# Performance work log

Measured on AMD Instinct MI355X. Metric: run time of the kernel, lower is better.

## Reference

```python
import jax, jax.numpy as jnp
import numpy as np

N_CELL, N_TISSUE, H, NH = 200000, 2000, 256, 8
HD = H // NH
SCALE = HD ** -0.5
EPS = 1e-5


def _layernorm(x, g, b):
    m = jnp.mean(x, axis=-1, keepdims=True)
    v = jnp.mean((x - m) ** 2, axis=-1, keepdims=True)
    return (x - m) / jnp.sqrt(v + EPS) * g + b


def setup_inputs() -> dict:
    key = jax.random.key(0)
    ks = jax.random.split(key, 12)
    s = 0.02

    def lin(k):
        k1, k2 = jax.random.split(k)
        return (jax.random.normal(k1, (H, H), jnp.float32) * s,
                jax.random.normal(k2, (H,), jnp.float32) * s)

    Wq_bu, bq_bu = lin(ks[0])
    Wk_bu, bk_bu = lin(ks[1])
    Wv_bu, bv_bu = lin(ks[2])
    Wo_bu, bo_bu = lin(ks[3])
    Wv_td, bv_td = lin(ks[4])
    Wo_td, bo_td = lin(ks[5])
    return dict(
        cell_features=jax.random.normal(ks[6], (N_CELL, H), jnp.float32),
        tissue_features=jax.random.normal(ks[7], (N_TISSUE, H), jnp.float32),
        cluster_labels=jax.random.randint(ks[8], (N_CELL,), 0, N_TISSUE, dtype=jnp.int32),
        tissue_batch=jnp.zeros((N_TISSUE,), jnp.int32),
        Wq_bu=Wq_bu, bq_bu=bq_bu, Wk_bu=Wk_bu, bk_bu=bk_bu,
        Wv_bu=Wv_bu, bv_bu=bv_bu, Wo_bu=Wo_bu, bo_bu=bo_bu,
        Wv_td=Wv_td, bv_td=bv_td, Wo_td=Wo_td, bo_td=bo_td,
        ln_cell_g=jnp.ones((H,), jnp.float32), ln_cell_b=jnp.zeros((H,), jnp.float32),
        ln_tissue_g=jnp.ones((H,), jnp.float32), ln_tissue_b=jnp.zeros((H,), jnp.float32),
    )


def reference(cell_features, tissue_features, cluster_labels, tissue_batch,
              Wq_bu, bq_bu, Wk_bu, bk_bu, Wv_bu, bv_bu, Wo_bu, bo_bu,
              Wv_td, bv_td, Wo_td, bo_td,
              ln_cell_g, ln_cell_b, ln_tissue_g, ln_tissue_b):
    Nc = cell_features.shape[0]
    Nt = tissue_features.shape[0]

    # ---- bottom-up: each tissue node (1 query) attends over its cells (segment attention) ----
    Q = (tissue_features @ Wq_bu + bq_bu).reshape(Nt, NH, HD)   # [Nt, h, d]
    K = (cell_features @ Wk_bu + bk_bu).reshape(Nc, NH, HD)     # [Nc, h, d]
    V = (cell_features @ Wv_bu + bv_bu).reshape(Nc, NH, HD)     # [Nc, h, d]

    # per-cell score against its own cluster's tissue query
    scores = jnp.einsum('nhd,nhd->nh', K, Q[cluster_labels]) * SCALE  # [Nc, h]
    smax = jax.lax.stop_gradient(
        jax.ops.segment_max(scores, cluster_labels, num_segments=Nt))  # [Nt, h]
    ex = jnp.exp(scores - smax[cluster_labels])
    denom = jax.ops.segment_sum(ex, cluster_labels, num_segments=Nt)   # [Nt, h]
    w = ex / denom[cluster_labels]                                     # [Nc, h]
    attended = jax.ops.segment_sum(w[..., None] * V, cluster_labels,
                                   num_segments=Nt)                    # [Nt, h, d]
    attended = attended.reshape(Nt, H) @ Wo_bu + bo_bu

    counts = jax.ops.segment_sum(jnp.ones((Nc,), cell_features.dtype),
                                 cluster_labels, num_segments=Nt)
    tissue_updated = jnp.where(counts[:, None] > 0, attended, tissue_features)

    # ---- top-down: each cell attends to its single tissue token ----
    # softmax over a single key is identically 1, so q/k projections cancel:
    # attended_cell = out_proj(v_proj(tissue_updated[cluster]))
    td_per_tissue = (tissue_updated @ Wv_td + bv_td) @ Wo_td + bo_td   # [Nt, H]
    cell_updated = td_per_tissue[cluster_labels]                       # [Nc, H]

    cell_out = _layernorm(cell_features + cell_updated, ln_cell_g, ln_cell_b)
    tissue_out = _layernorm(tissue_features + tissue_updated, ln_tissue_g, ln_tissue_b)
    return (cell_out, tissue_out)
```

## Files before the change

### kernel.cpp

```cpp
#include <hip/hip_runtime.h>
#include <math.h>

#define NC 200000
#define NT 2000
#define HH 256
#define NH_ 8
#define SCALE 0.17677669529663687f
#define EPS 1e-5f
#define SLICE 128
#define PSLICES (NT + NC / SLICE + 1)
#define PSTRIDE 2056


__global__ void k_hist(const int* __restrict__ labels, int* __restrict__ counts) {
  int i = blockIdx.x * 256 + threadIdx.x;
  if (i < NC) atomicAdd(&counts[labels[i]], 1);
}

__global__ void k_scan(const int* __restrict__ counts, int* __restrict__ offsets,
                       int* __restrict__ soff, int* __restrict__ slice_t) {
  int tid = threadIdx.x;
  int base = tid * 32;
  int la[32], lb[32], scnt[32];
  int sa = 0, sb = 0;
  #pragma unroll
  for (int k = 0; k < 32; k++) {
    int idx = base + k;
    int v = (idx < NT) ? counts[idx] : 0;
    la[k] = sa; lb[k] = sb;
    scnt[k] = (v + SLICE - 1) / SLICE;
    sa += v; sb += scnt[k];
  }
  int ia_ = sa, ib_ = sb;
  #pragma unroll
  for (int d = 1; d < 64; d <<= 1) {
    int oa = __shfl_up(ia_, d, 64);
    int ob = __shfl_up(ib_, d, 64);
    if (tid >= d) { ia_ += oa; ib_ += ob; }
  }
  int ea = ia_ - sa, eb = ib_ - sb;
  #pragma unroll
  for (int k = 0; k < 32; k++) {
    int idx = base + k;
    if (idx < NT) {
      offsets[idx] = ea + la[k];
      soff[idx] = eb + lb[k];
      int st = eb + lb[k];
      for (int s2 = 0; s2 < scnt[k]; s2++) slice_t[st + s2] = idx;
    }
  }
  if (tid == 63) { offsets[NT] = ia_; soff[NT] = ib_; }
}

__global__ void k_scatter(const int* __restrict__ labels, const int* __restrict__ offsets,
                          int* __restrict__ cursor, int* __restrict__ cindex) {
  int i = blockIdx.x * 256 + threadIdx.x;
  if (i < NC) {
    int c = labels[i];
    int pos = offsets[c] + atomicAdd(&cursor[c], 1);
    cindex[pos] = i;
  }
}


__global__ __launch_bounds__(256) void k_gemm_bias(
    const float* __restrict__ A, const float* __restrict__ W,
    const float* __restrict__ bias, float* __restrict__ C, int M)
{
  __shared__ float Al[16][33];
  __shared__ float Wl[32][HH];
  int tid = threadIdx.x;
  int r0 = blockIdx.x * 16;
  float acc[16];
  #pragma unroll
  for (int r = 0; r < 16; r++) acc[r] = 0.f;
  for (int k0 = 0; k0 < HH; k0 += 32) {
    for (int e = tid; e < 16 * 32; e += 256) {
      int r = e >> 5, k = e & 31;
      int row = r0 + r;
      Al[r][k] = (row < M) ? A[(size_t)row * HH + k0 + k] : 0.f;
    }
    for (int e = tid; e < 32 * HH; e += 256) {
      int k = e >> 8, j = e & 255;
      Wl[k][j] = W[(size_t)(k0 + k) * HH + j];
    }
    __syncthreads();
    for (int k = 0; k < 32; k++) {
      float w = Wl[k][tid];
      #pragma unroll
      for (int r = 0; r < 16; r++) acc[r] += Al[r][k] * w;
    }
    __syncthreads();
  }
  float bj = bias[tid];
  #pragma unroll
  for (int r = 0; r < 16; r++) {
    int row = r0 + r;
    if (row < M) C[(size_t)row * HH + tid] = acc[r] + bj;
  }
}


__global__ __launch_bounds__(256) void k_qproj(
    const float* __restrict__ Q, const float* __restrict__ Wk,
    const float* __restrict__ bk, float* __restrict__ Qproj,
    float* __restrict__ bkq)
{
  __shared__ float Al[64][33];
  __shared__ float Bl[32][257];
  int h = blockIdx.x & 7, tb = blockIdx.x >> 3;
  int t0 = tb * 64;
  int tid = threadIdx.x;
  for (int e = tid; e < 64 * 32; e += 256) {
    int r = e >> 5, d = e & 31;
    int t = t0 + r;
    Al[r][d] = (t < NT) ? Q[(size_t)t * HH + h * 32 + d] * SCALE : 0.f;
  }
  for (int e = tid; e < 256 * 32; e += 256) {
    int j = e >> 5, d = e & 31;
    Bl[d][j] = Wk[(size_t)j * HH + h * 32 + d];
  }
  __syncthreads();
  float acc[64];
  #pragma unroll
  for (int r = 0; r < 64; r++) acc[r] = 0.f;
  for (int d = 0; d < 32; d++) {
    float b = Bl[d][tid];
    #pragma unroll
    for (int r = 0; r < 64; r++) acc[r] += Al[r][d] * b;
  }
  for (int r = 0; r < 64; r++) {
    int t = t0 + r;
    if (t < NT) Qproj[((size_t)t * NH_ + h) * HH + tid] = acc[r];
  }
  if (tid < 64) {
    int t = t0 + tid;
    if (t < NT) {
      float s = 0.f;
      #pragma unroll
      for (int d = 0; d < 32; d++) s += Al[tid][d] * bk[h * 32 + d];
      bkq[t * NH_ + h] = s;
    }
  }
}


__global__ __launch_bounds__(256) void k_cellslice(
    const float* __restrict__ cell, const int* __restrict__ cindex,
    const int* __restrict__ offsets, const int* __restrict__ soff,
    const int* __restrict__ slice_t,
    const float* __restrict__ Qproj, const float* __restrict__ bkq,
    float* __restrict__ Pbuf)
{
  __shared__ float qp[NH_][HH];
  __shared__ float e_lds[SLICE][NH_];
  __shared__ int   cidx[SLICE];
  __shared__ float cwlds[NH_][HH];
  __shared__ float red[4][NH_];
  __shared__ float bqs[NH_];

  int s = blockIdx.x;
  if (s >= soff[NT]) return;
  int t = slice_t[s];
  int l = s - soff[t];
  int c0 = offsets[t] + l * SLICE;
  int c1 = min(c0 + SLICE, offsets[t + 1]);
  int nc = c1 - c0;
  int ncp = (nc + 15) & ~15;

  int tid = threadIdx.x;
  int w = tid >> 6, lane = tid & 63, slot = lane >> 3, g = lane & 7;

  for (int e = tid; e < NH_ * HH / 4; e += 256)
    ((float4*)qp)[e] = ((const float4*)(Qproj + (size_t)t * NH_ * HH))[e];
  if (tid < SLICE) cidx[tid] = cindex[min(c0 + tid, c1 - 1)];
  if (tid < NH_) bqs[tid] = bkq[t * NH_ + tid];
  for (int e = tid; e < SLICE * NH_; e += 256) ((float*)e_lds)[e] = 0.f;
  __syncthreads();

  int nsweep = ncp >> 4;
  for (int j = w; j < nsweep; j += 4) {
    int ia = j * 16 + slot, ib = ia + 8;
    const float* rowa = cell + (size_t)cidx[ia] * HH + g * 4;
    const float* rowb = cell + (size_t)cidx[ib] * HH + g * 4;
    float pa[NH_], pb[NH_];
    #pragma unroll
    for (int h = 0; h < NH_; h++) { pa[h] = 0.f; pb[h] = 0.f; }
    float4 a0 = *reinterpret_cast<const float4*>(rowa);
    float4 b0 = *reinterpret_cast<const float4*>(rowb);
    #pragma unroll
    for (int k = 0; k < 8; k++) {
      float4 a1, b1;
      if (k < 7) {
        a1 = *reinterpret_cast<const float4*>(rowa + 32 * (k + 1));
        b1 = *reinterpret_cast<const float4*>(rowb + 32 * (k + 1));
      }
      #pragma unroll
      for (int h = 0; h < NH_; h++) {
        float4 q = *reinterpret_cast<const float4*>(&qp[h][g * 4 + 32 * k]);
        pa[h] += a0.x * q.x + a0.y * q.y + a0.z * q.z + a0.w * q.w;
        pb[h] += b0.x * q.x + b0.y * q.y + b0.z * q.z + b0.w * q.w;
      }
      a0 = a1; b0 = b1;
    }
    #pragma unroll
    for (int d = 1; d < 8; d <<= 1) {
      #pragma unroll
      for (int h = 0; h < NH_; h++) {
        pa[h] += __shfl_xor(pa[h], d, 64);
        pb[h] += __shfl_xor(pb[h], d, 64);
      }
    }
    if (g == 0) {
      if (ia < nc) {
        float ea[NH_];
        #pragma unroll
        for (int h = 0; h < NH_; h++) ea[h] = __expf(pa[h] + bqs[h]);
        *reinterpret_cast<float4*>(&e_lds[ia][0]) = make_float4(ea[0], ea[1], ea[2], ea[3]);
        *reinterpret_cast<float4*>(&e_lds[ia][4]) = make_float4(ea[4], ea[5], ea[6], ea[7]);
      }
      if (ib < nc) {
        float eb[NH_];
        #pragma unroll
        for (int h = 0; h < NH_; h++) eb[h] = __expf(pb[h] + bqs[h]);
        *reinterpret_cast<float4*>(&e_lds[ib][0]) = make_float4(eb[0], eb[1], eb[2], eb[3]);
        *reinterpret_cast<float4*>(&e_lds[ib][4]) = make_float4(eb[4], eb[5], eb[6], eb[7]);
      }
    }
  }
  __syncthreads();

  float cw[NH_][4];
  float dsum[NH_];
  #pragma unroll
  for (int h = 0; h < NH_; h++) {
    cw[h][0] = cw[h][1] = cw[h][2] = cw[h][3] = 0.f;
    dsum[h] = 0.f;
  }
  for (int i = w * 4; i < ncp; i += 16) {
    float4 xx[4];
    #pragma unroll
    for (int c = 0; c < 4; c++)
      xx[c] = *reinterpret_cast<const float4*>(&cell[(size_t)cidx[i + c] * HH + lane * 4]);
    #pragma unroll
    for (int c = 0; c < 4; c++) {
      float4 e0 = *reinterpret_cast<float4*>(&e_lds[i + c][0]);
      float4 e1 = *reinterpret_cast<float4*>(&e_lds[i + c][4]);
      float4 x = xx[c];
      cw[0][0] += e0.x * x.x; cw[0][1] += e0.x * x.y; cw[0][2] += e0.x * x.z; cw[0][3] += e0.x * x.w;
      cw[1][0] += e0.y * x.x; cw[1][1] += e0.y * x.y; cw[1][2] += e0.y * x.z; cw[1][3] += e0.y * x.w;
      cw[2][0] += e0.z * x.x; cw[2][1] += e0.z * x.y; cw[2][2] += e0.z * x.z; cw[2][3] += e0.z * x.w;
      cw[3][0] += e0.w * x.x; cw[3][1] += e0.w * x.y; cw[3][2] += e0.w * x.z; cw[3][3] += e0.w * x.w;
      cw[4][0] += e1.x * x.x; cw[4][1] += e1.x * x.y; cw[4][2] += e1.x * x.z; cw[4][3] += e1.x * x.w;
      cw[5][0] += e1.y * x.x; cw[5][1] += e1.y * x.y; cw[5][2] += e1.y * x.z; cw[5][3] += e1.y * x.w;
      cw[6][0] += e1.z * x.x; cw[6][1] += e1.z * x.y; cw[6][2] += e1.z * x.z; cw[6][3] += e1.z * x.w;
      cw[7][0] += e1.w * x.x; cw[7][1] += e1.w * x.y; cw[7][2] += e1.w * x.z; cw[7][3] += e1.w * x.w;
      dsum[0] += e0.x; dsum[1] += e0.y; dsum[2] += e0.z; dsum[3] += e0.w;
      dsum[4] += e1.x; dsum[5] += e1.y; dsum[6] += e1.z; dsum[7] += e1.w;
    }
  }
  if (lane == 0) {
    #pragma unroll
    for (int h = 0; h < NH_; h++) red[w][h] = dsum[h];
  }
  if (w == 0) {
    #pragma unroll
    for (int h = 0; h < NH_; h++)
      *reinterpret_cast<float4*>(&cwlds[h][lane * 4]) =
          make_float4(cw[h][0], cw[h][1], cw[h][2], cw[h][3]);
  }
  __syncthreads();
  #pragma unroll
  for (int ww = 1; ww < 4; ww++) {
    if (w == ww) {
      #pragma unroll
      for (int h = 0; h < NH_; h++) {
        float4 c = *reinterpret_cast<float4*>(&cwlds[h][lane * 4]);
        c.x += cw[h][0]; c.y += cw[h][1]; c.z += cw[h][2]; c.w += cw[h][3];
        *reinterpret_cast<float4*>(&cwlds[h][lane * 4]) = c;
      }
    }
    __syncthreads();
  }

  float* pb = Pbuf + (size_t)s * PSTRIDE;
  #pragma unroll
  for (int h = 0; h < NH_; h++) pb[h * HH + tid] = cwlds[h][tid];
  if (tid < NH_) pb[2048 + tid] = red[0][tid] + red[1][tid] + red[2][tid] + red[3][tid];
}


#define TCH 4

__global__ __launch_bounds__(256) void k_tissuechain(
    const float* __restrict__ tissue, const int* __restrict__ counts,
    const float* __restrict__ Pbuf, const int* __restrict__ soff,
    const float* __restrict__ Wv, const float* __restrict__ bv,
    const float* __restrict__ Wo, const float* __restrict__ bo,
    const float* __restrict__ Wvtd, const float* __restrict__ bvtd,
    const float* __restrict__ Wotd, const float* __restrict__ botd,
    const float* __restrict__ lng, const float* __restrict__ lnb,
    float* __restrict__ td, float* __restrict__ out_tissue)
{
  __shared__ float s_cwn[TCH][NH_ * HH];
  __shared__ float s_a[TCH][HH];
  __shared__ float s_tu[TCH][HH];
  __shared__ float s_tmp[TCH][HH];
  __shared__ float s_red[2][4];
  __shared__ float s_dinv[TCH][NH_];
  int t0 = blockIdx.x * TCH;
  int j = threadIdx.x;
  int h = j >> 5;

  if (j < TCH * NH_) {
    int t = j >> 3, hh = j & 7;
    int s0 = soff[t0 + t], s1 = soff[t0 + t + 1];
    float d = 0.f;
    for (int q = s0; q < s1; q++) d += Pbuf[(size_t)q * PSTRIDE + 2048 + hh];
    s_dinv[t][hh] = (s1 > s0) ? 1.f / d : 0.f;
  }
  __syncthreads();

  for (int e = j; e < TCH * NH_ * HH; e += 256) {
    int t = e >> 11, c = e & 2047, hh = c >> 8;
    int s0 = soff[t0 + t], s1 = soff[t0 + t + 1];
    float a = 0.f;
    for (int q = s0; q < s1; q++) a += Pbuf[(size_t)q * PSTRIDE + c];
    s_cwn[t][c] = a * s_dinv[t][hh];
  }
  __syncthreads();

  float acc[TCH];
  #pragma unroll
  for (int t = 0; t < TCH; t++) acc[t] = 0.f;
  for (int k = 0; k < HH; k++) {
    float w = Wv[(size_t)k * HH + j];
    #pragma unroll
    for (int t = 0; t < TCH; t++) acc[t] += s_cwn[t][h * HH + k] * w;
  }
  {
    float bj = bv[j];
    #pragma unroll
    for (int t = 0; t < TCH; t++) s_a[t][j] = acc[t] + bj;
  }
  __syncthreads();

  #pragma unroll
  for (int t = 0; t < TCH; t++) acc[t] = 0.f;
  for (int k = 0; k < HH; k++) {
    float w = Wo[(size_t)k * HH + j];
    #pragma unroll
    for (int t = 0; t < TCH; t++) acc[t] += s_a[t][k] * w;
  }
  {
    float bj = bo[j];
    #pragma unroll
    for (int t = 0; t < TCH; t++) {
      int tt = t0 + t;
      s_tu[t][j] = (counts[tt] > 0) ? (acc[t] + bj) : tissue[(size_t)tt * HH + j];
    }
  }
  __syncthreads();

  #pragma unroll
  for (int t = 0; t < TCH; t++) acc[t] = 0.f;
  for (int k = 0; k < HH; k++) {
    float w = Wvtd[(size_t)k * HH + j];
    #pragma unroll
    for (int t = 0; t < TCH; t++) acc[t] += s_tu[t][k] * w;
  }
  {
    float bj = bvtd[j];
    #pragma unroll
    for (int t = 0; t < TCH; t++) s_tmp[t][j] = acc[t] + bj;
  }
  __syncthreads();

  #pragma unroll
  for (int t = 0; t < TCH; t++) acc[t] = 0.f;
  for (int k = 0; k < HH; k++) {
    float w = Wotd[(size_t)k * HH + j];
    #pragma unroll
    for (int t = 0; t < TCH; t++) acc[t] += s_tmp[t][k] * w;
  }
  {
    float bj = botd[j];
    #pragma unroll
    for (int t = 0; t < TCH; t++) td[(size_t)(t0 + t) * HH + j] = acc[t] + bj;
  }

  float gj = lng[j], bj2 = lnb[j];
  for (int t = 0; t < TCH; t++) {
    float y = tissue[(size_t)(t0 + t) * HH + j] + s_tu[t][j];
    float s1 = y, s2 = y * y;
    #pragma unroll
    for (int d = 1; d < 64; d <<= 1) { s1 += __shfl_xor(s1, d, 64); s2 += __shfl_xor(s2, d, 64); }
    int wv_ = j >> 6, ln_ = j & 63;
    __syncthreads();
    if (ln_ == 0) { s_red[0][wv_] = s1; s_red[1][wv_] = s2; }
    __syncthreads();
    s1 = s_red[0][0] + s_red[0][1] + s_red[0][2] + s_red[0][3];
    s2 = s_red[1][0] + s_red[1][1] + s_red[1][2] + s_red[1][3];
    float mean = s1 * (1.f / 256.f);
    float var = s2 * (1.f / 256.f) - mean * mean;
    float inv = rsqrtf(var + EPS);
    out_tissue[(size_t)(t0 + t) * HH + j] = (y - mean) * inv * gj + bj2;
  }
}


#define COB 2048

__global__ __launch_bounds__(256) void k_cellout(
    const float* __restrict__ cell, const float* __restrict__ td,
    const int* __restrict__ labels,
    const float* __restrict__ lng, const float* __restrict__ lnb,
    float* __restrict__ out)
{
  int lane = threadIdx.x & 63;
  float4 gv = *reinterpret_cast<const float4*>(&lng[lane * 4]);
  float4 bv = *reinterpret_cast<const float4*>(&lnb[lane * 4]);
  int wid = blockIdx.x * 4 + (threadIdx.x >> 6);
  for (int row = wid; row < NC; row += COB * 4) {
    int c = labels[row];
    float4 x = *reinterpret_cast<const float4*>(&cell[(size_t)row * HH + lane * 4]);
    float4 u = *reinterpret_cast<const float4*>(&td[(size_t)c * HH + lane * 4]);
    float y0 = x.x + u.x, y1 = x.y + u.y, y2 = x.z + u.z, y3 = x.w + u.w;
    float s1 = y0 + y1 + y2 + y3;
    float s2 = y0 * y0 + y1 * y1 + y2 * y2 + y3 * y3;
    #pragma unroll
    for (int d = 1; d < 64; d <<= 1) { s1 += __shfl_xor(s1, d, 64); s2 += __shfl_xor(s2, d, 64); }
    float mean = s1 * (1.f / 256.f);
    float var = s2 * (1.f / 256.f) - mean * mean;
    float inv = rsqrtf(var + EPS);
    float4 o;
    o.x = (y0 - mean) * inv * gv.x + bv.x;
    o.y = (y1 - mean) * inv * gv.y + bv.y;
    o.z = (y2 - mean) * inv * gv.z + bv.z;
    o.w = (y3 - mean) * inv * gv.w + bv.w;
    *reinterpret_cast<float4*>(&out[(size_t)row * HH + lane * 4]) = o;
  }
}


extern "C" void kernel_launch(void* const* d_in, const int* in_sizes, int n_in,
                              void* d_out, int out_size, void* d_ws, size_t ws_size,
                              hipStream_t stream) {
  const float* cell   = (const float*)d_in[0];
  const float* tissue = (const float*)d_in[1];
  const int*   labels = (const int*)d_in[2];
  const float* Wq = (const float*)d_in[4];  const float* bq = (const float*)d_in[5];
  const float* Wk = (const float*)d_in[6];  const float* bk = (const float*)d_in[7];
  const float* Wv = (const float*)d_in[8];  const float* bv = (const float*)d_in[9];
  const float* Wo = (const float*)d_in[10]; const float* bo = (const float*)d_in[11];
  const float* Wvtd = (const float*)d_in[12]; const float* bvtd = (const float*)d_in[13];
  const float* Wotd = (const float*)d_in[14]; const float* botd = (const float*)d_in[15];
  const float* lncg = (const float*)d_in[16]; const float* lncb = (const float*)d_in[17];
  const float* lntg = (const float*)d_in[18]; const float* lntb = (const float*)d_in[19];
  float* out_cell   = (float*)d_out;
  float* out_tissue = (float*)d_out + (size_t)NC * HH;

  char* w = (char*)d_ws;
  auto take = [&](size_t bytes) { void* p = (void*)w; w += (bytes + 255) & ~(size_t)255; return p; };
  int*   counts  = (int*)take((size_t)NT * 4);
  int*   cursor  = (int*)take((size_t)NT * 4);
  int*   offsets = (int*)take((size_t)(NT + 1) * 4);
  int*   soff    = (int*)take((size_t)(NT + 1) * 4);
  int*   slice_t = (int*)take((size_t)PSLICES * 4);
  int*   cindex  = (int*)take((size_t)NC * 4);
  float* Q       = (float*)take((size_t)NT * HH * 4);
  float* Qproj   = (float*)take((size_t)NT * NH_ * HH * 4);
  float* bkq     = (float*)take((size_t)NT * NH_ * 4);
  float* td      = (float*)take((size_t)NT * HH * 4);
  float* Pbuf    = (float*)take((size_t)PSLICES * PSTRIDE * 4);

  hipMemsetAsync(counts, 0, 16384, stream);

  const int CB = (NC + 255) / 256;
  k_hist<<<CB, 256, 0, stream>>>(labels, counts);
  k_scan<<<1, 64, 0, stream>>>(counts, offsets, soff, slice_t);
  k_scatter<<<CB, 256, 0, stream>>>(labels, offsets, cursor, cindex);

  k_gemm_bias<<<(NT + 15) / 16, 256, 0, stream>>>(tissue, Wq, bq, Q, NT);
  k_qproj<<<8 * ((NT + 63) / 64), 256, 0, stream>>>(Q, Wk, bk, Qproj, bkq);

  k_cellslice<<<PSLICES, 256, 0, stream>>>(cell, cindex, offsets, soff, slice_t,
                                           Qproj, bkq, Pbuf);

  k_tissuechain<<<NT / TCH, 256, 0, stream>>>(tissue, counts, Pbuf, soff,
      Wv, bv, Wo, bo, Wvtd, bvtd, Wotd, botd, lntg, lntb, td, out_tissue);

  k_cellout<<<COB, 256, 0, stream>>>(cell, td, labels, lncg, lncb, out_cell);
}
```

Baseline: 457.1 us.

## Fuse score and weighted-sum passes in cell slice kernel into one pass

```diff
diff --git a/kernel.cpp b/kernel.cpp
--- a/kernel.cpp
+++ b/kernel.cpp
@@ -152,12 +152,9 @@
     const float* __restrict__ Qproj, const float* __restrict__ bkq,
     float* __restrict__ Pbuf)
 {
-  __shared__ float qp[NH_][HH];
-  __shared__ float e_lds[SLICE][NH_];
   __shared__ int   cidx[SLICE];
   __shared__ float cwlds[NH_][HH];
   __shared__ float red[4][NH_];
-  __shared__ float bqs[NH_];
 
   int s = blockIdx.x;
   if (s >= soff[NT]) return;
@@ -166,118 +163,95 @@
   int c0 = offsets[t] + l * SLICE;
   int c1 = min(c0 + SLICE, offsets[t + 1]);
   int nc = c1 - c0;
-  int ncp = (nc + 15) & ~15;
+  int ncp = (nc + 3) & ~3;
 
   int tid = threadIdx.x;
-  int w = tid >> 6, lane = tid & 63, slot = lane >> 3, g = lane & 7;
-
-  for (int e = tid; e < NH_ * HH / 4; e += 256)
-    ((float4*)qp)[e] = ((const float4*)(Qproj + (size_t)t * NH_ * HH))[e];
+  int w = tid >> 6, lane = tid & 63;
+  int hg = lane & 3, kc = lane >> 2;
+
   if (tid < SLICE) cidx[tid] = cindex[min(c0 + tid, c1 - 1)];
-  if (tid < NH_) bqs[tid] = bkq[t * NH_ + tid];
-  for (int e = tid; e < SLICE * NH_; e += 256) ((float*)e_lds)[e] = 0.f;
-  __syncthreads();
-
-  int nsweep = ncp >> 4;
-  for (int j = w; j < nsweep; j += 4) {
-    int ia = j * 16 + slot, ib = ia + 8;
-    const float* rowa = cell + (size_t)cidx[ia] * HH + g * 4;
-    const float* rowb = cell + (size_t)cidx[ib] * HH + g * 4;
-    float pa[NH_], pb[NH_];
-    #pragma unroll
-    for (int h = 0; h < NH_; h++) { pa[h] = 0.f; pb[h] = 0.f; }
-    float4 a0 = *reinterpret_cast<const float4*>(rowa);
-    float4 b0 = *reinterpret_cast<const float4*>(rowb);
-    #pragma unroll
-    for (int k = 0; k < 8; k++) {
-      float4 a1, b1;
-      if (k < 7) {
-        a1 = *reinterpret_cast<const float4*>(rowa + 32 * (k + 1));
-        b1 = *reinterpret_cast<const float4*>(rowb + 32 * (k + 1));
-      }
-      #pragma unroll
-      for (int h = 0; h < NH_; h++) {
-        float4 q = *reinterpret_cast<const float4*>(&qp[h][g * 4 + 32 * k]);
-        pa[h] += a0.x * q.x + a0.y * q.y + a0.z * q.z + a0.w * q.w;
-        pb[h] += b0.x * q.x + b0.y * q.y + b0.z * q.z + b0.w * q.w;
-      }
-      a0 = a1; b0 = b1;
-    }
-    #pragma unroll
-    for (int d = 1; d < 8; d <<= 1) {
-      #pragma unroll
-      for (int h = 0; h < NH_; h++) {
-        pa[h] += __shfl_xor(pa[h], d, 64);
-        pb[h] += __shfl_xor(pb[h], d, 64);
-      }
-    }
-    if (g == 0) {
-      if (ia < nc) {
-        float ea[NH_];
-        #pragma unroll
-        for (int h = 0; h < NH_; h++) ea[h] = __expf(pa[h] + bqs[h]);
-        *reinterpret_cast<float4*>(&e_lds[ia][0]) = make_float4(ea[0], ea[1], ea[2], ea[3]);
-        *reinterpret_cast<float4*>(&e_lds[ia][4]) = make_float4(ea[4], ea[5], ea[6], ea[7]);
-      }
-      if (ib < nc) {
-        float eb[NH_];
-        #pragma unroll
-        for (int h = 0; h < NH_; h++) eb[h] = __expf(pb[h] + bqs[h]);
-        *reinterpret_cast<float4*>(&e_lds[ib][0]) = make_float4(eb[0], eb[1], eb[2], eb[3]);
-        *reinterpret_cast<float4*>(&e_lds[ib][4]) = make_float4(eb[4], eb[5], eb[6], eb[7]);
-      }
-    }
-  }
-  __syncthreads();
-
-  float cw[NH_][4];
-  float dsum[NH_];
-  #pragma unroll
-  for (int h = 0; h < NH_; h++) {
-    cw[h][0] = cw[h][1] = cw[h][2] = cw[h][3] = 0.f;
-    dsum[h] = 0.f;
-  }
-  for (int i = w * 4; i < ncp; i += 16) {
-    float4 xx[4];
-    #pragma unroll
-    for (int c = 0; c < 4; c++)
-      xx[c] = *reinterpret_cast<const float4*>(&cell[(size_t)cidx[i + c] * HH + lane * 4]);
-    #pragma unroll
-    for (int c = 0; c < 4; c++) {
-      float4 e0 = *reinterpret_cast<float4*>(&e_lds[i + c][0]);
-      float4 e1 = *reinterpret_cast<float4*>(&e_lds[i + c][4]);
-      float4 x = xx[c];
-      cw[0][0] += e0.x * x.x; cw[0][1] += e0.x * x.y; cw[0][2] += e0.x * x.z; cw[0][3] += e0.x * x.w;
-      cw[1][0] += e0.y * x.x; cw[1][1] += e0.y * x.y; cw[1][2] += e0.y * x.z; cw[1][3] += e0.y * x.w;
-      cw[2][0] += e0.z * x.x; cw[2][1] += e0.z * x.y; cw[2][2] += e0.z * x.z; cw[2][3] += e0.z * x.w;
-      cw[3][0] += e0.w * x.x; cw[3][1] += e0.w * x.y; cw[3][2] += e0.w * x.z; cw[3][3] += e0.w * x.w;
-      cw[4][0] += e1.x * x.x; cw[4][1] += e1.x * x.y; cw[4][2] += e1.x * x.z; cw[4][3] += e1.x * x.w;
-      cw[5][0] += e1.y * x.x; cw[5][1] += e1.y * x.y; cw[5][2] += e1.y * x.z; cw[5][3] += e1.y * x.w;
-      cw[6][0] += e1.z * x.x; cw[6][1] += e1.z * x.y; cw[6][2] += e1.z * x.z; cw[6][3] += e1.z * x.w;
-      cw[7][0] += e1.w * x.x; cw[7][1] += e1.w * x.y; cw[7][2] += e1.w * x.z; cw[7][3] += e1.w * x.w;
-      dsum[0] += e0.x; dsum[1] += e0.y; dsum[2] += e0.z; dsum[3] += e0.w;
-      dsum[4] += e1.x; dsum[5] += e1.y; dsum[6] += e1.z; dsum[7] += e1.w;
-    }
-  }
-  if (lane == 0) {
-    #pragma unroll
-    for (int h = 0; h < NH_; h++) red[w][h] = dsum[h];
-  }
+
+  const float* qpb = Qproj + (size_t)t * NH_ * HH;
+  float4 qp0[4], qp1[4];
+  #pragma unroll
+  for (int i = 0; i < 4; i++) {
+    qp0[i] = *reinterpret_cast<const float4*>(qpb + (2 * hg) * HH + (i * 16 + kc) * 4);
+    qp1[i] = *reinterpret_cast<const float4*>(qpb + (2 * hg + 1) * HH + (i * 16 + kc) * 4);
+  }
+  float bq0 = bkq[t * NH_ + 2 * hg];
+  float bq1 = bkq[t * NH_ + 2 * hg + 1];
+
+  float4 cw0[4], cw1[4];
+  #pragma unroll
+  for (int i = 0; i < 4; i++) {
+    cw0[i] = make_float4(0.f, 0.f, 0.f, 0.f);
+    cw1[i] = make_float4(0.f, 0.f, 0.f, 0.f);
+  }
+  float d0 = 0.f, d1 = 0.f;
+
+  __syncthreads();
+
+  float4 x[4], xn[4];
+  {
+    const float* r = cell + (size_t)cidx[min(w, nc - 1)] * HH;
+    #pragma unroll
+    for (int i = 0; i < 4; i++)
+      x[i] = *reinterpret_cast<const float4*>(r + (i * 16 + kc) * 4);
+  }
+
+  for (int ic = w; ic < ncp; ic += 4) {
+    int icn = min(ic + 4, nc - 1);
+    const float* rn = cell + (size_t)cidx[icn] * HH;
+    #pragma unroll
+    for (int i = 0; i < 4; i++)
+      xn[i] = *reinterpret_cast<const float4*>(rn + (i * 16 + kc) * 4);
+
+    float s0 = 0.f, s1 = 0.f;
+    #pragma unroll
+    for (int i = 0; i < 4; i++) {
+      s0 += x[i].x * qp0[i].x + x[i].y * qp0[i].y + x[i].z * qp0[i].z + x[i].w * qp0[i].w;
+      s1 += x[i].x * qp1[i].x + x[i].y * qp1[i].y + x[i].z * qp1[i].z + x[i].w * qp1[i].w;
+    }
+    #pragma unroll
+    for (int d = 4; d < 64; d <<= 1) {
+      s0 += __shfl_xor(s0, d, 64);
+      s1 += __shfl_xor(s1, d, 64);
+    }
+    float e0 = __expf(s0 + bq0);
+    float e1 = __expf(s1 + bq1);
+    if (ic >= nc) { e0 = 0.f; e1 = 0.f; }
+    d0 += e0; d1 += e1;
+    #pragma unroll
+    for (int i = 0; i < 4; i++) {
+      cw0[i].x += e0 * x[i].x; cw0[i].y += e0 * x[i].y;
+      cw0[i].z += e0 * x[i].z; cw0[i].w += e0 * x[i].w;
+      cw1[i].x += e1 * x[i].x; cw1[i].y += e1 * x[i].y;
+      cw1[i].z += e1 * x[i].z; cw1[i].w += e1 * x[i].w;
+    }
+    #pragma unroll
+    for (int i = 0; i < 4; i++) x[i] = xn[i];
+  }
+
   if (w == 0) {
     #pragma unroll
-    for (int h = 0; h < NH_; h++)
-      *reinterpret_cast<float4*>(&cwlds[h][lane * 4]) =
-          make_float4(cw[h][0], cw[h][1], cw[h][2], cw[h][3]);
-  }
+    for (int i = 0; i < 4; i++) {
+      *reinterpret_cast<float4*>(&cwlds[2 * hg][(i * 16 + kc) * 4]) = cw0[i];
+      *reinterpret_cast<float4*>(&cwlds[2 * hg + 1][(i * 16 + kc) * 4]) = cw1[i];
+    }
+  }
+  if (kc == 0) { red[w][2 * hg] = d0; red[w][2 * hg + 1] = d1; }
   __syncthreads();
   #pragma unroll
   for (int ww = 1; ww < 4; ww++) {
     if (w == ww) {
       #pragma unroll
-      for (int h = 0; h < NH_; h++) {
-        float4 c = *reinterpret_cast<float4*>(&cwlds[h][lane * 4]);
-        c.x += cw[h][0]; c.y += cw[h][1]; c.z += cw[h][2]; c.w += cw[h][3];
-        *reinterpret_cast<float4*>(&cwlds[h][lane * 4]) = c;
+      for (int i = 0; i < 4; i++) {
+        float4 a = *reinterpret_cast<float4*>(&cwlds[2 * hg][(i * 16 + kc) * 4]);
+        a.x += cw0[i].x; a.y += cw0[i].y; a.z += cw0[i].z; a.w += cw0[i].w;
+        *reinterpret_cast<float4*>(&cwlds[2 * hg][(i * 16 + kc) * 4]) = a;
+        float4 b = *reinterpret_cast<float4*>(&cwlds[2 * hg + 1][(i * 16 + kc) * 4]);
+        b.x += cw1[i].x; b.y += cw1[i].y; b.z += cw1[i].z; b.w += cw1[i].w;
+        *reinterpret_cast<float4*>(&cwlds[2 * hg + 1][(i * 16 + kc) * 4]) = b;
       }
     }
     __syncthreads();
```

Result: faster. 405.0 us (-11.4%).
